# Performance work log

Hardware: AMD Instinct MI355X
Metric: run time of the kernel (lower is better)

## Reference

```python
import jax, jax.numpy as jnp
import numpy as np

B, NP, J, C, H, W, L = 16, 64, 17, 480, 128, 128, 4
EPS = 1e-5
COCO_EDGES = [(15,13),(13,11),(16,14),(14,12),(11,12),(5,11),(6,12),(5,6),(5,7),(6,8),(7,9),(8,10),(1,2),(0,1),(0,2),(1,3),(2,4),(3,5),(4,6)]

def build_adj():
    g = np.eye(J, dtype=np.float32)
    for a, b in COCO_EDGES:
        g[a, b] = 1.0
        g[b, a] = 1.0
    r = g.sum(1) ** -0.5  # symmetric normalization D^-1/2 A D^-1/2
    return jnp.asarray(r[:, None] * g * r[None, :])

def make_bn(k):
    ks = jax.random.split(k, 4)
    gamma = 1.0 + 0.1 * jax.random.normal(ks[0], (C,))
    beta = 0.1 * jax.random.normal(ks[1], (C,))
    mean = 0.1 * jax.random.normal(ks[2], (C,))
    var = 0.5 + jax.random.uniform(ks[3], (C,))
    return jnp.stack([gamma, beta, mean, var])  # [4, C]

def setup_inputs() -> dict:
    key = jax.random.key(0)
    ks = jax.random.split(key, 12)
    s = 0.02
    features = jax.random.normal(ks[0], (B, C, H, W), jnp.float32)
    coords = jax.random.uniform(ks[1], (B, NP, J, 2)) * jnp.array([W - 1.0, H - 1.0], jnp.float32)
    center_ind = jax.random.randint(ks[2], (B, NP), 0, H * W)
    bn_res = jax.vmap(make_bn)(jax.random.split(ks[3], L * 2)).reshape(L, 2, 4, C)
    return {
        'features': features,
        'coords': coords,
        'center_ind': center_ind,
        'adj': build_adj(),
        'Wh': s * jax.random.normal(ks[4], (C, C)),
        'bh': jnp.zeros((C,)),
        'bn_head': make_bn(ks[5]),
        'Wres': s * jax.random.normal(ks[6], (L, 2, C, C)),
        'bres': jnp.zeros((L, 2, C)),
        'bn_res': bn_res,
        'Wp1': s * jax.random.normal(ks[7], (C, 3 * C)),
        'bp1': jnp.zeros((C,)),
        'bn_pred': make_bn(ks[8]),
        'Wp2': s * jax.random.normal(ks[9], (2 * J, C)),
        'bp2': jnp.zeros((2 * J,)),
    }

def _bn(x, p):
    # eval-mode BatchNorm1d over the channel (last) axis; p = [gamma, beta, mean, var]
    return (x - p[2]) * jax.lax.rsqrt(p[3] + EPS) * p[0] + p[1]

def _gblock(x, adj, Wt, bt, p):
    # graph conv (adj @ (x W) + b) -> BN -> ReLU ; x: [N, J, C]
    return jax.nn.relu(_bn(jnp.einsum('jk,nkc->njc', adj, x @ Wt) + bt, p))

_gat = jax.vmap(lambda f, i: f[:, i])  # f: [C, HW], i: int idx -> [C, *i.shape]

def reference(features, coords, center_ind, adj, Wh, bh, bn_head, Wres, bres, bn_res, Wp1, bp1, bn_pred, Wp2, bp2):
    flat = features.reshape(B, C, H * W)
    # --- float_sample: bilinear sampling of per-joint features ---
    x, y = coords[..., 0], coords[..., 1]
    x0f = jnp.clip(jnp.floor(x), 0.0, W - 2.0)
    y0f = jnp.clip(jnp.floor(y), 0.0, H - 2.0)
    x0 = x0f.astype(jnp.int32)
    y0 = y0f.astype(jnp.int32)
    wx = (x - x0f)[:, None]  # [B,1,NP,J]
    wy = (y - y0f)[:, None]
    i00 = y0 * W + x0
    f00 = _gat(flat, i00)
    f01 = _gat(flat, i00 + 1)
    f10 = _gat(flat, i00 + W)
    f11 = _gat(flat, i00 + W + 1)
    fj = f00 * (1 - wx) * (1 - wy) + f01 * wx * (1 - wy) + f10 * (1 - wx) * wy + f11 * wx * wy  # [B,C,NP,J]
    feat_joints = jnp.transpose(fj, (0, 2, 3, 1)).reshape(B * NP, J, C)
    # --- int_sample: center features ---
    feat_center = jnp.transpose(_gat(flat, center_ind), (0, 2, 1))  # [B,NP,C]
    # --- stacked graph conv blocks ---
    h = _gblock(feat_joints, adj, Wh, bh, bn_head)
    for i in range(L):
        res = h
        h = _gblock(h, adj, Wres[i, 0], bres[i, 0], bn_res[i, 0])
        h = _gblock(h, adj, Wres[i, 1], bres[i, 1], bn_res[i, 1])
        h = res + h
    f1 = h.mean(axis=1).reshape(B, NP, C)
    f2 = h.max(axis=1).reshape(B, NP, C)
    feats = jnp.concatenate([f1, f2, feat_center], axis=-1)  # [B,NP,3C]
    p = jax.nn.relu(_bn(feats @ Wp1.T + bp1, bn_pred))  # 1x1 conv + BN + ReLU
    return p @ Wp2.T + bp2  # [B, NP, 2*J] refine offsets
```

## Files before the change

### kernel.cpp

```cpp
#include <hip/hip_runtime.h>
#include <math.h>

#define B_    16
#define NP_   64
#define J_    17
#define C_    480
#define H_    128
#define W_    128
#define L_    4
#define HW_   (H_ * W_)
#define NSAMP (B_ * NP_)
#define MROWS (NSAMP * J_)
#define EPS_  1e-5f
#define NMAT  (1 + 2 * L_)
#define NPAD  512
#define TC    96
#define TS    64
#define NT_   (256 * 5 * B_)
#define NW_   11520

typedef __attribute__((ext_vector_type(8))) short bf16x8;
typedef __attribute__((ext_vector_type(4))) short bf16x4;
typedef __attribute__((ext_vector_type(4))) float f32x4;

__device__ __forceinline__ unsigned short f2bf(float f) {
    unsigned int u = __float_as_uint(f);
    unsigned int r = (u + 0x7fffu + ((u >> 16) & 1u)) >> 16;
    return (unsigned short)r;
}
__device__ __forceinline__ float bf2f(unsigned short h) {
    return __uint_as_float(((unsigned int)h) << 16);
}

#define GLD16(gsrc, ldst)                                                                 \
    __builtin_amdgcn_global_load_lds((const __attribute__((address_space(1))) void*)(gsrc), \
                                     (__attribute__((address_space(3))) void*)(ldst), 16, 0, 0)

__global__ __launch_bounds__(256) void k_prep(const float* __restrict__ feat,
                                              const float* __restrict__ Wh,
                                              const float* __restrict__ Wres,
                                              const float* __restrict__ Wp1,
                                              short* __restrict__ nhwc,
                                              short* __restrict__ WtH,
                                              short* __restrict__ WpH) {
    int bid = blockIdx.x;
    int tid = threadIdx.x;
    if (bid < NT_) {
        __shared__ float t[TC][73];
        int sb = bid & 255;
        int cb = (bid >> 8) % 5;
        int b  = bid / 1280;
        int c0 = cb * TC, s0 = sb * TS;
        const float* src = feat + ((size_t)b * C_ + c0) * HW_ + s0;
        #pragma unroll
        for (int i = 0; i < 6; ++i) {
            int f  = tid + i * 256;
            int c  = f >> 4;
            int sq = (f & 15) * 4;
            float4 v = *reinterpret_cast<const float4*>(src + (size_t)c * HW_ + sq);
            t[c][sq + 0] = v.x;
            t[c][sq + 1] = v.y;
            t[c][sq + 2] = v.z;
            t[c][sq + 3] = v.w;
        }
        __syncthreads();
        int sy = tid >> 2;
        int cx = (tid & 3) * (TC / 4);
        short* dst = nhwc + ((size_t)b * HW_ + s0 + sy) * C_ + c0 + cx;
        alignas(16) unsigned short tmp[TC / 4];
        #pragma unroll
        for (int i = 0; i < TC / 4; ++i) tmp[i] = f2bf(t[cx + i][sy]);
        #pragma unroll
        for (int i = 0; i < 3; ++i)
            *reinterpret_cast<uint4*>(dst + i * 8) = *reinterpret_cast<const uint4*>(tmp + i * 8);
    } else {
        int gid = (bid - NT_) * 256 + tid;
        const int t1 = NMAT * NPAD * C_;
        const int t2 = NPAD * 3 * C_;
        if (gid < t1) {
            int m   = gid / (NPAD * C_);
            int rem = gid % (NPAD * C_);
            int n = rem / C_;
            int k = rem % C_;
            float v = 0.f;
            if (n < C_) {
                const float* src = (m == 0) ? Wh : (Wres + (size_t)(m - 1) * C_ * C_);
                v = src[(size_t)k * C_ + n];
            }
            WtH[gid] = (short)f2bf(v);
        } else if (gid < t1 + t2) {
            int g2 = gid - t1;
            int n = g2 / (3 * C_);
            int k = g2 % (3 * C_);
            float v = (n < C_) ? Wp1[(size_t)n * 3 * C_ + k] : 0.f;
            WpH[g2] = (short)f2bf(v);
        }
    }
}

__global__ __launch_bounds__(256) void k_gather_mix(const short* __restrict__ nhwc,
                                                    const float* __restrict__ coords,
                                                    const float* __restrict__ adj,
                                                    short* __restrict__ Ah) {
    __shared__ float sX[J_][C_];
    __shared__ float sadj[J_ * J_];
    __shared__ float sw[J_][4];
    __shared__ int   si[J_];
    int n = blockIdx.x;
    int b = n / NP_;
    for (int t = threadIdx.x; t < J_ * J_; t += 256) sadj[t] = adj[t];
    if (threadIdx.x < J_) {
        int j = threadIdx.x;
        int p = n * J_ + j;
        float x = coords[p * 2 + 0];
        float y = coords[p * 2 + 1];
        float x0f = fminf(fmaxf(floorf(x), 0.f), (float)(W_ - 2));
        float y0f = fminf(fmaxf(floorf(y), 0.f), (float)(H_ - 2));
        float wx = x - x0f, wy = y - y0f;
        sw[j][0] = (1.f - wx) * (1.f - wy);
        sw[j][1] = wx * (1.f - wy);
        sw[j][2] = (1.f - wx) * wy;
        sw[j][3] = wx * wy;
        si[j] = (int)y0f * W_ + (int)x0f;
    }
    __syncthreads();
    const short* base = nhwc + (size_t)b * HW_ * C_;
    for (int idx = threadIdx.x; idx < J_ * (C_ / 8); idx += 256) {
        int j  = idx / (C_ / 8);
        int c8 = (idx - j * (C_ / 8)) * 8;
        const short* p00 = base + (size_t)si[j] * C_ + c8;
        bf16x8 v00 = *reinterpret_cast<const bf16x8*>(p00);
        bf16x8 v01 = *reinterpret_cast<const bf16x8*>(p00 + C_);
        bf16x8 v10 = *reinterpret_cast<const bf16x8*>(p00 + W_ * C_);
        bf16x8 v11 = *reinterpret_cast<const bf16x8*>(p00 + W_ * C_ + C_);
        float w0 = sw[j][0], w1 = sw[j][1], w2 = sw[j][2], w3 = sw[j][3];
        #pragma unroll
        for (int e = 0; e < 8; ++e) {
            sX[j][c8 + e] = bf2f((unsigned short)v00[e]) * w0 +
                            bf2f((unsigned short)v01[e]) * w1 +
                            bf2f((unsigned short)v10[e]) * w2 +
                            bf2f((unsigned short)v11[e]) * w3;
        }
    }
    __syncthreads();
    size_t obase = (size_t)n * J_ * C_;
    for (int c = threadIdx.x; c < C_; c += 256) {
        float xv[J_];
        #pragma unroll
        for (int k = 0; k < J_; k++) xv[k] = sX[k][c];
        #pragma unroll
        for (int j = 0; j < J_; j++) {
            float s = 0.f;
            #pragma unroll
            for (int k = 0; k < J_; k++) s += sadj[j * J_ + k] * xv[k];
            Ah[obase + (size_t)j * C_ + c] = (short)f2bf(s);
        }
    }
}

__global__ __launch_bounds__(256) void k_mix_bf16(const short* __restrict__ Xin,
                                                  const float* __restrict__ adj,
                                                  short* __restrict__ Ah) {
    __shared__ float sadj[J_ * J_];
    for (int t = threadIdx.x; t < J_ * J_; t += 256) sadj[t] = adj[t];
    __syncthreads();
    int t = threadIdx.x;
    if (t >= 240) return;
    int n  = blockIdx.x * 2 + (t / 120);
    int c4 = (t % 120) * 4;
    const short* xb = Xin + (size_t)n * J_ * C_ + c4;
    float xf[J_][4];
    #pragma unroll
    for (int k = 0; k < J_; k++) {
        bf16x4 v = *reinterpret_cast<const bf16x4*>(xb + (size_t)k * C_);
        #pragma unroll
        for (int e = 0; e < 4; ++e) xf[k][e] = bf2f((unsigned short)v[e]);
    }
    short* yb = Ah + (size_t)n * J_ * C_ + c4;
    #pragma unroll
    for (int j = 0; j < J_; j++) {
        float a0 = 0.f, a1 = 0.f, a2 = 0.f, a3 = 0.f;
        #pragma unroll
        for (int k = 0; k < J_; k++) {
            float w = sadj[j * J_ + k];
            a0 = fmaf(w, xf[k][0], a0);
            a1 = fmaf(w, xf[k][1], a1);
            a2 = fmaf(w, xf[k][2], a2);
            a3 = fmaf(w, xf[k][3], a3);
        }
        bf16x4 o = {(short)f2bf(a0), (short)f2bf(a1), (short)f2bf(a2), (short)f2bf(a3)};
        *reinterpret_cast<bf16x4*>(yb + (size_t)j * C_) = o;
    }
}

template <bool ADD>
__global__ __launch_bounds__(256) void k_gemm_mfma(const short* __restrict__ A,
                                                   const short* __restrict__ Bm,
                                                   const float* __restrict__ bias,
                                                   const float* __restrict__ bn4,
                                                   const short* res,
                                                   short* out,
                                                   int M, int N, int K) {
    __shared__ short lds[2 * 2 * 4096];

    int nwg = gridDim.x * gridDim.y;
    int lin = blockIdx.y * gridDim.x + blockIdx.x;
    int cpx = nwg >> 3;
    int swz = (lin & 7) * cpx + (lin >> 3);
    const int row0 = (swz / gridDim.x) * 128;
    const int col0 = (swz % gridDim.x) * 128;

    const int tid  = threadIdx.x;
    const int lane = tid & 63;
    const int wid  = tid >> 6;
    const int wm0  = (wid >> 1) * 64;
    const int wn0  = (wid & 1) * 64;

    f32x4 acc[4][4];
    #pragma unroll
    for (int i = 0; i < 4; i++)
        #pragma unroll
        for (int j = 0; j < 4; j++) acc[i][j] = (f32x4){0.f, 0.f, 0.f, 0.f};

    const int kq = lane >> 4;
    const int fr = lane & 15;

    int r_[2], cq_[2];
    #pragma unroll
    for (int t = 0; t < 2; ++t) {
        int p = (2 * wid + t) * 1024 + lane * 16;
        int v = p >> 6;
        int r = v ^ ((v >> 2) & 1);
        r_[t]  = r;
        cq_[t] = ((p >> 4) & 3) ^ (r & 3);
    }
    const short* pA0 = A  + (size_t)(row0 + r_[0]) * K + cq_[0] * 8;
    const short* pA1 = A  + (size_t)(row0 + r_[1]) * K + cq_[1] * 8;
    const short* pB0 = Bm + (size_t)(col0 + r_[0]) * K + cq_[0] * 8;
    const short* pB1 = Bm + (size_t)(col0 + r_[1]) * K + cq_[1] * 8;
    const int a0 = (2 * wid + 0) * 1024;
    const int a1 = (2 * wid + 1) * 1024;

    const int NS = K / 32;
    {
        char* lb = (char*)lds;
        GLD16(pA0, lb + a0);        GLD16(pA1, lb + a1);
        GLD16(pB0, lb + 8192 + a0); GLD16(pB1, lb + 8192 + a1);
    }
    __syncthreads();

    for (int ks = 0; ks < NS; ++ks) {
        if (ks + 1 < NS) {
            const int kk = (ks + 1) * 32;
            char* lb = (char*)lds + ((ks + 1) & 1) * 16384;
            GLD16(pA0 + kk, lb + a0);        GLD16(pA1 + kk, lb + a1);
            GLD16(pB0 + kk, lb + 8192 + a0); GLD16(pB1 + kk, lb + 8192 + a1);
        }
        const short* lbc = lds + (ks & 1) * 8192;
        bf16x8 fa[4], fb[4];
        #pragma unroll
        for (int mf = 0; mf < 4; ++mf) {
            int r  = wm0 + mf * 16 + fr;
            int so = ((r * 64 + kq * 16) ^ ((r & 7) << 4)) >> 1;
            fa[mf] = *reinterpret_cast<const bf16x8*>(lbc + so);
        }
        #pragma unroll
        for (int nf = 0; nf < 4; ++nf) {
            int r  = wn0 + nf * 16 + fr;
            int so = ((r * 64 + kq * 16) ^ ((r & 7) << 4)) >> 1;
            fb[nf] = *reinterpret_cast<const bf16x8*>(lbc + 4096 + so);
        }
        __builtin_amdgcn_s_setprio(1);
        #pragma unroll
        for (int mf = 0; mf < 4; ++mf)
            #pragma unroll
            for (int nf = 0; nf < 4; ++nf)
                acc[mf][nf] = __builtin_amdgcn_mfma_f32_16x16x32_bf16(fa[mf], fb[nf], acc[mf][nf], 0, 0, 0);
        __builtin_amdgcn_s_setprio(0);
        __syncthreads();
    }

    const int rq = lane >> 4;
    #pragma unroll
    for (int nf = 0; nf < 4; ++nf) {
        int col = col0 + wn0 + nf * 16 + fr;
        if (col >= N) continue;
        float bia = bias[col];
        float g   = bn4[col];
        float be  = bn4[N + col];
        float mu  = bn4[2 * N + col];
        float va  = bn4[3 * N + col];
        float sc  = rsqrtf(va + EPS_) * g;
        #pragma unroll
        for (int mf = 0; mf < 4; ++mf) {
            #pragma unroll
            for (int r = 0; r < 4; ++r) {
                int row = row0 + wm0 + mf * 16 + rq * 4 + r;
                float v = acc[mf][nf][r] + bia;
                v = (v - mu) * sc + be;
                v = fmaxf(v, 0.f);
                if (ADD) v += bf2f((unsigned short)res[(size_t)row * N + col]);
                out[(size_t)row * N + col] = (short)f2bf(v);
            }
        }
    }
}

__global__ __launch_bounds__(256) void k_pool(const short* __restrict__ Hb,
                                              const short* __restrict__ nhwc,
                                              const int* __restrict__ cidx,
                                              short* __restrict__ feats) {
    int n = blockIdx.x;
    int b = n / NP_;
    const short* cen = nhwc + ((size_t)b * HW_ + cidx[n]) * C_;
    for (int c = threadIdx.x; c < C_; c += 256) {
        float s = 0.f, m = -INFINITY;
        #pragma unroll
        for (int j = 0; j < J_; j++) {
            float v = bf2f((unsigned short)Hb[((size_t)n * J_ + j) * C_ + c]);
            s += v;
            m = fmaxf(m, v);
        }
        feats[(size_t)n * 3 * C_ + c]          = (short)f2bf(s * (1.f / (float)J_));
        feats[(size_t)n * 3 * C_ + C_ + c]     = (short)f2bf(m);
        feats[(size_t)n * 3 * C_ + 2 * C_ + c] = cen[c];
    }
}

__global__ __launch_bounds__(256) void k_final(const short* __restrict__ P,
                                               const float* __restrict__ W2,
                                               const float* __restrict__ b2,
                                               float* __restrict__ out) {
    int g = blockIdx.x * 256 + threadIdx.x;
    if (g >= NSAMP * 2 * J_) return;
    int m = g / (2 * J_);
    int o = g % (2 * J_);
    const short* pr = P + (size_t)m * C_;
    const float* wr = W2 + (size_t)o * C_;
    float s = 0.f;
    for (int k = 0; k < C_; k += 4) {
        s = fmaf(bf2f((unsigned short)pr[k + 0]), wr[k + 0], s);
        s = fmaf(bf2f((unsigned short)pr[k + 1]), wr[k + 1], s);
        s = fmaf(bf2f((unsigned short)pr[k + 2]), wr[k + 2], s);
        s = fmaf(bf2f((unsigned short)pr[k + 3]), wr[k + 3], s);
    }
    out[g] = s + b2[o];
}

extern "C" void kernel_launch(void* const* d_in, const int* in_sizes, int n_in,
                              void* d_out, int out_size, void* d_ws, size_t ws_size,
                              hipStream_t stream) {
    const float* features = (const float*)d_in[0];
    const float* coords   = (const float*)d_in[1];
    const int*   center   = (const int*)d_in[2];
    const float* adj      = (const float*)d_in[3];
    const float* Wh       = (const float*)d_in[4];
    const float* bh       = (const float*)d_in[5];
    const float* bn_head  = (const float*)d_in[6];
    const float* Wres     = (const float*)d_in[7];
    const float* bres     = (const float*)d_in[8];
    const float* bn_res   = (const float*)d_in[9];
    const float* Wp1      = (const float*)d_in[10];
    const float* bp1      = (const float*)d_in[11];
    const float* bn_pred  = (const float*)d_in[12];
    const float* Wp2      = (const float*)d_in[13];
    const float* bp2      = (const float*)d_in[14];
    float* out = (float*)d_out;

    char* ws = (char*)d_ws;
    short* nhwc  = (short*)ws;   ws += (size_t)B_ * HW_ * C_ * 2;
    short* bufX  = (short*)ws;   ws += (size_t)MROWS * C_ * 2;
    short* bufH  = (short*)ws;   ws += (size_t)MROWS * C_ * 2;
    short* AhB   = (short*)ws;   ws += (size_t)MROWS * C_ * 2;
    short* featsB= (short*)ws;   ws += (size_t)NSAMP * 3 * C_ * 2;
    short* bufP  = (short*)ws;   ws += (size_t)NSAMP * C_ * 2;
    short* WtH   = (short*)ws;   ws += (size_t)NMAT * NPAD * C_ * 2;
    short* WpH   = (short*)ws;   ws += (size_t)NPAD * 3 * C_ * 2;

    dim3 gg(4, MROWS / 128);
    dim3 gp(4, NSAMP / 128);

    k_prep<<<NT_ + NW_, 256, 0, stream>>>(features, Wh, Wres, Wp1, nhwc, WtH, WpH);

    k_gather_mix<<<NSAMP, 256, 0, stream>>>(nhwc, coords, adj, AhB);
    k_gemm_mfma<false><<<gg, 256, 0, stream>>>(AhB, WtH, bh, bn_head,
                                               nullptr, bufH, MROWS, C_, C_);

    for (int i = 0; i < L_; i++) {
        int m1 = 1 + 2 * i, m2 = 2 + 2 * i;
        k_mix_bf16<<<NSAMP / 2, 256, 0, stream>>>(bufH, adj, AhB);
        k_gemm_mfma<false><<<gg, 256, 0, stream>>>(
            AhB, WtH + (size_t)m1 * NPAD * C_,
            bres + (size_t)(2 * i) * C_, bn_res + (size_t)(2 * i) * 4 * C_,
            nullptr, bufX, MROWS, C_, C_);
        k_mix_bf16<<<NSAMP / 2, 256, 0, stream>>>(bufX, adj, AhB);
        k_gemm_mfma<true><<<gg, 256, 0, stream>>>(
            AhB, WtH + (size_t)m2 * NPAD * C_,
            bres + (size_t)(2 * i + 1) * C_, bn_res + (size_t)(2 * i + 1) * 4 * C_,
            bufH, bufH, MROWS, C_, C_);
    }

    k_pool<<<NSAMP, 256, 0, stream>>>(bufH, nhwc, center, featsB);

    k_gemm_mfma<false><<<gp, 256, 0, stream>>>(featsB, WpH, bp1, bn_pred,
                                               nullptr, bufP, NSAMP, C_, 3 * C_);

    k_final<<<(NSAMP * 2 * J_ + 255) / 256, 256, 0, stream>>>(bufP, Wp2, bp2, out);
}
```

Baseline: 593.8 us.

## Switch GEMM to 32x32x16 MFMA with k-major LDS tile layout

```diff
diff --git a/kernel.cpp b/kernel.cpp
--- a/kernel.cpp
+++ b/kernel.cpp
@@ -21,7 +21,7 @@
 
 typedef __attribute__((ext_vector_type(8))) short bf16x8;
 typedef __attribute__((ext_vector_type(4))) short bf16x4;
-typedef __attribute__((ext_vector_type(4))) float f32x4;
+typedef __attribute__((ext_vector_type(16))) float f32x16;
 
 __device__ __forceinline__ unsigned short f2bf(float f) {
     unsigned int u = __float_as_uint(f);
@@ -215,29 +215,21 @@
     const int wid  = tid >> 6;
     const int wm0  = (wid >> 1) * 64;
     const int wn0  = (wid & 1) * 64;
-
-    f32x4 acc[4][4];
+    const int r31  = lane & 31;
+    const int oct  = lane >> 5;
+
+    f32x16 acc[2][2];
     #pragma unroll
-    for (int i = 0; i < 4; i++)
-        #pragma unroll
-        for (int j = 0; j < 4; j++) acc[i][j] = (f32x4){0.f, 0.f, 0.f, 0.f};
-
-    const int kq = lane >> 4;
-    const int fr = lane & 15;
-
-    int r_[2], cq_[2];
-    #pragma unroll
-    for (int t = 0; t < 2; ++t) {
-        int p = (2 * wid + t) * 1024 + lane * 16;
-        int v = p >> 6;
-        int r = v ^ ((v >> 2) & 1);
-        r_[t]  = r;
-        cq_[t] = ((p >> 4) & 3) ^ (r & 3);
-    }
-    const short* pA0 = A  + (size_t)(row0 + r_[0]) * K + cq_[0] * 8;
-    const short* pA1 = A  + (size_t)(row0 + r_[1]) * K + cq_[1] * 8;
-    const short* pB0 = Bm + (size_t)(col0 + r_[0]) * K + cq_[0] * 8;
-    const short* pB1 = Bm + (size_t)(col0 + r_[1]) * K + cq_[1] * 8;
+    for (int i = 0; i < 2; i++)
+        #pragma unroll
+        for (int j = 0; j < 2; j++)
+            #pragma unroll
+            for (int e = 0; e < 16; e++) acc[i][j][e] = 0.f;
+
+    const short* pA0 = A  + (size_t)(row0 + lane) * K + wid * 8;
+    const short* pA1 = A  + (size_t)(row0 + 64 + lane) * K + wid * 8;
+    const short* pB0 = Bm + (size_t)(col0 + lane) * K + wid * 8;
+    const short* pB1 = Bm + (size_t)(col0 + 64 + lane) * K + wid * 8;
     const int a0 = (2 * wid + 0) * 1024;
     const int a1 = (2 * wid + 1) * 1024;
 
@@ -257,33 +249,35 @@
             GLD16(pB0 + kk, lb + 8192 + a0); GLD16(pB1 + kk, lb + 8192 + a1);
         }
         const short* lbc = lds + (ks & 1) * 8192;
-        bf16x8 fa[4], fb[4];
-        #pragma unroll
-        for (int mf = 0; mf < 4; ++mf) {
-            int r  = wm0 + mf * 16 + fr;
-            int so = ((r * 64 + kq * 16) ^ ((r & 7) << 4)) >> 1;
-            fa[mf] = *reinterpret_cast<const bf16x8*>(lbc + so);
-        }
-        #pragma unroll
-        for (int nf = 0; nf < 4; ++nf) {
-            int r  = wn0 + nf * 16 + fr;
-            int so = ((r * 64 + kq * 16) ^ ((r & 7) << 4)) >> 1;
-            fb[nf] = *reinterpret_cast<const bf16x8*>(lbc + 4096 + so);
-        }
+        bf16x8 fa[2][2], fb[2][2];
+        #pragma unroll
+        for (int mf = 0; mf < 2; ++mf)
+            #pragma unroll
+            for (int kf = 0; kf < 2; ++kf)
+                fa[mf][kf] = *reinterpret_cast<const bf16x8*>(
+                    lbc + (kf * 2 + oct) * 1024 + (wm0 + mf * 32 + r31) * 8);
+        #pragma unroll
+        for (int nf = 0; nf < 2; ++nf)
+            #pragma unroll
+            for (int kf = 0; kf < 2; ++kf)
+                fb[nf][kf] = *reinterpret_cast<const bf16x8*>(
+                    lbc + 4096 + (kf * 2 + oct) * 1024 + (wn0 + nf * 32 + r31) * 8);
         __builtin_amdgcn_s_setprio(1);
         #pragma unroll
-        for (int mf = 0; mf < 4; ++mf)
-            #pragma unroll
-            for (int nf = 0; nf < 4; ++nf)
-                acc[mf][nf] = __builtin_amdgcn_mfma_f32_16x16x32_bf16(fa[mf], fb[nf], acc[mf][nf], 0, 0, 0);
+        for (int mf = 0; mf < 2; ++mf)
+            #pragma unroll
+            for (int nf = 0; nf < 2; ++nf)
+                #pragma unroll
+                for (int kf = 0; kf < 2; ++kf)
+                    acc[mf][nf] = __builtin_amdgcn_mfma_f32_32x32x16_bf16(
+                        fa[mf][kf], fb[nf][kf], acc[mf][nf], 0, 0, 0);
         __builtin_amdgcn_s_setprio(0);
         __syncthreads();
     }
 
-    const int rq = lane >> 4;
     #pragma unroll
-    for (int nf = 0; nf < 4; ++nf) {
-        int col = col0 + wn0 + nf * 16 + fr;
+    for (int nf = 0; nf < 2; ++nf) {
+        int col = col0 + wn0 + nf * 32 + r31;
         if (col >= N) continue;
         float bia = bias[col];
         float g   = bn4[col];
@@ -292,11 +286,12 @@
         float va  = bn4[3 * N + col];
         float sc  = rsqrtf(va + EPS_) * g;
         #pragma unroll
-        for (int mf = 0; mf < 4; ++mf) {
-            #pragma unroll
-            for (int r = 0; r < 4; ++r) {
-                int row = row0 + wm0 + mf * 16 + rq * 4 + r;
-                float v = acc[mf][nf][r] + bia;
+        for (int mf = 0; mf < 2; ++mf) {
+            int rbase = row0 + wm0 + mf * 32 + 4 * oct;
+            #pragma unroll
+            for (int reg = 0; reg < 16; ++reg) {
+                int row = rbase + (reg & 3) + 8 * (reg >> 2);
+                float v = acc[mf][nf][reg] + bia;
                 v = (v - mu) * sc + be;
                 v = fmaxf(v, 0.f);
                 if (ADD) v += bf2f((unsigned short)res[(size_t)row * N + col]);
```

Result: slower. 702.7 us (+18.3%).
